# Kernel tuning notes

Hardware: AMD Instinct MI355X
Metric: run time of the kernel (lower is better)

Reference implementation:

```python
import jax, jax.numpy as jnp
import numpy as np

N_HEAD = 16
N_KV = 4
HEAD_DIM = 128
N_EMBD = 2048
GATE_CH = 32


def setup_inputs() -> dict:
    key = jax.random.key(0)
    ks = jax.random.split(key, 9)
    B, T = 2, 2048
    return {
        "x": jax.random.normal(ks[0], (B, T, N_EMBD), jnp.float32),
        "ve": jax.random.normal(ks[1], (B, T, N_KV * HEAD_DIM), jnp.float32),
        "cos": jax.random.uniform(ks[2], (T, 1, HEAD_DIM // 2), jnp.float32),
        "sin": jax.random.uniform(ks[3], (T, 1, HEAD_DIM // 2), jnp.float32),
        "wq": jax.random.normal(ks[4], (N_HEAD * HEAD_DIM, N_EMBD), jnp.float32) * 0.02,
        "wk": jax.random.normal(ks[5], (N_KV * HEAD_DIM, N_EMBD), jnp.float32) * 0.02,
        "wv": jax.random.normal(ks[6], (N_KV * HEAD_DIM, N_EMBD), jnp.float32) * 0.02,
        "wo": jax.random.normal(ks[7], (N_EMBD, N_EMBD), jnp.float32) * 0.02,
        "wgate": jax.random.normal(ks[8], (N_KV, GATE_CH), jnp.float32) * 0.02,
        "window_size": 512,
    }


def _rope(t, cos, sin):
    half = t.shape[-1] // 2
    t1, t2 = t[..., :half], t[..., half:]
    return jnp.concatenate([t1 * cos + t2 * sin, -t1 * sin + t2 * cos], axis=-1)


def _rms(t):
    eps = jnp.finfo(t.dtype).eps
    return t * jax.lax.rsqrt(jnp.mean(t * t, axis=-1, keepdims=True) + eps)


def reference(x, ve, cos, sin, wq, wk, wv, wo, wgate, window_size):
    B, T, _ = x.shape
    q = (x @ wq.T).reshape(B, T, N_HEAD, HEAD_DIM)
    k = (x @ wk.T).reshape(B, T, N_KV, HEAD_DIM)
    v = (x @ wv.T).reshape(B, T, N_KV, HEAD_DIM)
    # value-embedding gate
    gate = 2.0 * jax.nn.sigmoid(x[..., :GATE_CH] @ wgate.T)  # [B,T,N_KV]
    v = v + gate[..., None] * ve.reshape(B, T, N_KV, HEAD_DIM)
    # RoPE then QK RMSNorm
    q = _rms(_rope(q, cos, sin)).transpose(0, 2, 1, 3)  # [B,H,T,D]
    k = _rms(_rope(k, cos, sin)).transpose(0, 2, 1, 3)  # [B,KV,T,D]
    v = v.transpose(0, 2, 1, 3)
    rep = N_HEAD // N_KV
    k = jnp.repeat(k, rep, axis=1)  # repeat_interleave over head dim
    v = jnp.repeat(v, rep, axis=1)
    # sliding-window causal mask (past_len=0, key_len=T)
    pos = jnp.arange(T)
    mask = (pos[None, :] <= pos[:, None]) & (pos[None, :] >= pos[:, None] - window_size + 1)
    scale = 1.0 / jnp.sqrt(jnp.float32(HEAD_DIM))
    scores = jnp.einsum("bhqd,bhkd->bhqk", q, k) * scale
    scores = jnp.where(mask[None, None], scores, jnp.finfo(scores.dtype).min)
    attn = jax.nn.softmax(scores, axis=-1)
    y = jnp.einsum("bhqk,bhkd->bhqd", attn, v)
    y = y.transpose(0, 2, 1, 3).reshape(B, T, N_EMBD)
    return y @ wo.T
```

## Files before the change

kernel.cpp:

```cpp
#include <hip/hip_runtime.h>
#include <hip/hip_bf16.h>

typedef __attribute__((ext_vector_type(8))) short short8_t;
typedef __attribute__((ext_vector_type(4))) float f32x4;
typedef __attribute__((ext_vector_type(16))) float f32x16;
using bf16 = __hip_bfloat16;

#define MFMA_BF16(A, B, C) __builtin_amdgcn_mfma_f32_16x16x32_bf16((A), (B), (C), 0, 0, 0)
#define MFMA32_BF16(A, B, C) __builtin_amdgcn_mfma_f32_32x32x16_bf16((A), (B), (C), 0, 0, 0)

#define GLD_LDS16(g, l)                                                        \
  __builtin_amdgcn_global_load_lds(                                           \
      (const __attribute__((address_space(1))) unsigned int*)(const void*)(g),\
      (__attribute__((address_space(3))) unsigned int*)(void*)(l), 16, 0, 0)

__device__ __forceinline__ float bits2f(short s) {
  union { unsigned int u; float f; } c;
  c.u = ((unsigned int)(unsigned short)s) << 16;
  return c.f;
}
__device__ __forceinline__ short f2bits(float f) {
  bf16 h = __float2bfloat16(f);
  return *reinterpret_cast<short*>(&h);
}
__device__ __forceinline__ unsigned pack2(float lo, float hi) {
  return ((unsigned)(unsigned short)f2bits(lo)) |
         (((unsigned)(unsigned short)f2bits(hi)) << 16);
}
__device__ __forceinline__ float exp2_(float x) {
#if __has_builtin(__builtin_amdgcn_exp2f)
  return __builtin_amdgcn_exp2f(x);
#else
  return exp2f(x);
#endif
}

__global__ __launch_bounds__(256) void cvt_all(const float* __restrict__ x,
                                               const float* __restrict__ wq,
                                               const float* __restrict__ wk,
                                               const float* __restrict__ wv,
                                               const float* __restrict__ wo,
                                               short* __restrict__ xb,
                                               short* __restrict__ wqkvb,
                                               short* __restrict__ wob) {
  int i = (blockIdx.x * 256 + threadIdx.x) * 4;
  const float* src;
  short* dst;
  if (i < 8388608) {
    src = x + i; dst = xb + i;
  } else if (i < 14680064) {
    int j = i - 8388608;
    dst = wqkvb + j;
    if (j < 4194304) src = wq + j;
    else if (j < 5242880) src = wk + (j - 4194304);
    else src = wv + (j - 5242880);
  } else {
    int j = i - 14680064;
    src = wo + j; dst = wob + j;
  }
  float4 v = *reinterpret_cast<const float4*>(src);
  short4 o;
  o.x = f2bits(v.x); o.y = f2bits(v.y); o.z = f2bits(v.z); o.w = f2bits(v.w);
  *reinterpret_cast<short4*>(dst) = o;
}

template <int STORE_BF16>
__global__ __launch_bounds__(256, 2) void gemm_bt4(const short* __restrict__ A,
                                                   const short* __restrict__ Bt,
                                                   void* __restrict__ C,
                                                   int M, int N, int K,
                                                   int CM, int CN) {
  __shared__ __align__(16) short lds[2 * 16384];
  const int c = (int)blockIdx.x & 7;
  const int i = (int)blockIdx.x >> 3;
  const int cmi = c & 3, cni = c >> 2;
  const int m0 = (cmi * CM + (i % CM)) * 128;
  const int n0 = (cni * CN + (i / CM)) * 128;

  const int tid = threadIdx.x, w = tid >> 6, lane = tid & 63;
  const int wr = w >> 1, wc = w & 1;
  const int rr = lane & 15, g = lane >> 4;

  const int srow = tid >> 3;
  const int gc = (tid & 7) ^ (srow & 7);
  const short* Asrc = A + (size_t)(m0 + srow) * K + gc * 8;
  const short* Bsrc = Bt + (size_t)(n0 + srow) * K + gc * 8;
  const size_t rstep = (size_t)32 * K;
  const int dofs = tid * 16;

  const int abase = (((wr * 64 + rr) << 7) | (g << 4)) ^ ((rr & 7) << 4);
  const int bbase = ((((wc * 64 + rr) << 7) | (g << 4)) ^ ((rr & 7) << 4)) + 16384;

  f32x4 acc[4][4];
#pragma unroll
  for (int mi = 0; mi < 4; ++mi)
#pragma unroll
    for (int ni = 0; ni < 4; ++ni) acc[mi][ni] = (f32x4){0.f, 0.f, 0.f, 0.f};

  const int nt = K >> 6;

#define STAGE4(t, bufbyte) do {                                                \
    const short* a_ = Asrc + (size_t)(t) * 64;                                 \
    const short* b_ = Bsrc + (size_t)(t) * 64;                                 \
    char* la_ = (char*)lds + (bufbyte) + dofs;                                 \
    GLD_LDS16(a_,             la_);                                            \
    GLD_LDS16(a_ + rstep,     la_ + 4096);                                     \
    GLD_LDS16(a_ + 2 * rstep, la_ + 8192);                                     \
    GLD_LDS16(a_ + 3 * rstep, la_ + 12288);                                    \
    GLD_LDS16(b_,             la_ + 16384);                                    \
    GLD_LDS16(b_ + rstep,     la_ + 20480);                                    \
    GLD_LDS16(b_ + 2 * rstep, la_ + 24576);                                    \
    GLD_LDS16(b_ + 3 * rstep, la_ + 28672);                                    \
  } while (0)

  STAGE4(0, 0);
  asm volatile("s_waitcnt vmcnt(0)" ::: "memory");
  asm volatile("s_barrier" ::: "memory");

  int cur = 0;
  for (int t = 0; t < nt; ++t) {
    if (t + 1 < nt) STAGE4(t + 1, cur ^ 32768);
    const char* bufp = (const char*)lds + cur;
#pragma unroll
    for (int kk = 0; kk < 2; ++kk) {
      const int ko = kk * 64;
      short8_t a0 = *(const short8_t*)(bufp + ((abase ^ ko)));
      short8_t a1 = *(const short8_t*)(bufp + ((abase ^ ko) + 2048));
      short8_t a2 = *(const short8_t*)(bufp + ((abase ^ ko) + 4096));
      short8_t a3 = *(const short8_t*)(bufp + ((abase ^ ko) + 6144));
      short8_t b0 = *(const short8_t*)(bufp + ((bbase ^ ko)));
      short8_t b1 = *(const short8_t*)(bufp + ((bbase ^ ko) + 2048));
      short8_t b2 = *(const short8_t*)(bufp + ((bbase ^ ko) + 4096));
      short8_t b3 = *(const short8_t*)(bufp + ((bbase ^ ko) + 6144));
      __builtin_amdgcn_s_setprio(1);
      acc[0][0] = MFMA_BF16(a0, b0, acc[0][0]);
      acc[0][1] = MFMA_BF16(a0, b1, acc[0][1]);
      acc[0][2] = MFMA_BF16(a0, b2, acc[0][2]);
      acc[0][3] = MFMA_BF16(a0, b3, acc[0][3]);
      acc[1][0] = MFMA_BF16(a1, b0, acc[1][0]);
      acc[1][1] = MFMA_BF16(a1, b1, acc[1][1]);
      acc[1][2] = MFMA_BF16(a1, b2, acc[1][2]);
      acc[1][3] = MFMA_BF16(a1, b3, acc[1][3]);
      acc[2][0] = MFMA_BF16(a2, b0, acc[2][0]);
      acc[2][1] = MFMA_BF16(a2, b1, acc[2][1]);
      acc[2][2] = MFMA_BF16(a2, b2, acc[2][2]);
      acc[2][3] = MFMA_BF16(a2, b3, acc[2][3]);
      acc[3][0] = MFMA_BF16(a3, b0, acc[3][0]);
      acc[3][1] = MFMA_BF16(a3, b1, acc[3][1]);
      acc[3][2] = MFMA_BF16(a3, b2, acc[3][2]);
      acc[3][3] = MFMA_BF16(a3, b3, acc[3][3]);
      __builtin_amdgcn_s_setprio(0);
    }
    if (t + 1 < nt) {
      asm volatile("s_waitcnt vmcnt(0)" ::: "memory");
      asm volatile("s_barrier" ::: "memory");
    }
    cur ^= 32768;
  }
#undef STAGE4

#pragma unroll
  for (int mi = 0; mi < 4; ++mi)
#pragma unroll
    for (int ni = 0; ni < 4; ++ni) {
      const int row = m0 + wr * 64 + mi * 16 + g * 4;
      const int col = n0 + wc * 64 + ni * 16 + rr;
#pragma unroll
      for (int j = 0; j < 4; ++j) {
        float v = acc[mi][ni][j];
        if (STORE_BF16)
          reinterpret_cast<short*>(C)[(size_t)(row + j) * N + col] = f2bits(v);
        else
          reinterpret_cast<float*>(C)[(size_t)(row + j) * N + col] = v;
      }
    }
}

__global__ __launch_bounds__(256) void rope_rms_qk(const short* __restrict__ qkv,
                                                   const float* __restrict__ cosT,
                                                   const float* __restrict__ sinT,
                                                   short* __restrict__ qO,
                                                   short* __restrict__ kO) {
  const int T = 2048;
  int unit = blockIdx.x * 4 + (threadIdx.x >> 6);
  int lane = threadIdx.x & 63;
  int hh = unit % 20;
  int t = (unit / 20) % T;
  int b = unit / (20 * T);
  int col = hh < 16 ? hh * 128 : 2048 + (hh - 16) * 128;
  const short* src = qkv + (size_t)(b * T + t) * 3072 + col;
  float t1 = bits2f(src[lane]), t2 = bits2f(src[lane + 64]);
  float c = cosT[t * 64 + lane], s = sinT[t * 64 + lane];
  float o1 = t1 * c + t2 * s;
  float o2 = t2 * c - t1 * s;
  float ss = o1 * o1 + o2 * o2;
#pragma unroll
  for (int o = 1; o < 64; o <<= 1) ss += __shfl_xor(ss, o, 64);
  float r = rsqrtf(ss * (1.f / 128.f) + 1.1920929e-07f);
  short* dst;
  if (hh < 16) {
    r *= 0.08838834764831845f * 1.4426950408889634f;
    dst = qO + ((size_t)(b * 16 + hh) * T + t) * 128;
  } else {
    dst = kO + ((size_t)(b * 4 + (hh - 16)) * T + t) * 128;
  }
  dst[lane] = f2bits(o1 * r);
  dst[lane + 64] = f2bits(o2 * r);
}

__global__ __launch_bounds__(256) void vgate_t(const short* __restrict__ qkv,
                                               const float* __restrict__ x,
                                               const float* __restrict__ ve,
                                               const float* __restrict__ wgate,
                                               short* __restrict__ vT) {
  const int T = 2048;
  int bkv = blockIdx.x & 7;
  int t0 = (blockIdx.x >> 3) * 64;
  int b = bkv >> 2, kv = bkv & 3;
  __shared__ __align__(16) short L[128 * 64];
  int tid = threadIdx.x;
  int tt = tid >> 2, q = tid & 3;
  size_t m = (size_t)b * T + t0 + tt;
  float z = 0.f;
  const float* xp = x + m * 2048 + q * 8;
  const float* wgp = wgate + kv * 32 + q * 8;
#pragma unroll
  for (int i = 0; i < 8; ++i) z += xp[i] * wgp[i];
  z += __shfl_xor(z, 1, 64);
  z += __shfl_xor(z, 2, 64);
  float gate = 2.f / (1.f + __expf(-z));
  const short* vsrc = qkv + m * 3072 + 2560 + kv * 128 + q * 32;
  const float* vesrc = ve + m * 512 + kv * 128 + q * 32;
  short8_t v0 = *(const short8_t*)(vsrc);
  short8_t v1 = *(const short8_t*)(vsrc + 8);
  short8_t v2 = *(const short8_t*)(vsrc + 16);
  short8_t v3 = *(const short8_t*)(vsrc + 24);
  float4 e[8];
#pragma unroll
  for (int i = 0; i < 8; ++i) e[i] = *(const float4*)(vesrc + i * 4);
#pragma unroll
  for (int i = 0; i < 32; ++i) {
    int d = q * 32 + i;
    short vv = i < 8 ? v0[i] : i < 16 ? v1[i - 8] : i < 24 ? v2[i - 16] : v3[i - 24];
    float ev = (&e[i >> 2].x)[i & 3];
    int byte = (d * 128 + tt * 2) ^ ((d & 7) << 4);
    *(short*)((char*)L + byte) = f2bits(bits2f(vv) + gate * ev);
  }
  __syncthreads();
  int d = tid >> 1, th = tid & 1;
  const char* Lp = (const char*)L;
#pragma unroll
  for (int g2 = 0; g2 < 4; ++g2) {
    short8_t o = *(const short8_t*)(Lp + ((d * 128 + th * 64 + g2 * 16) ^ ((d & 7) << 4)));
    *(short8_t*)(vT + ((size_t)bkv * 128 + d) * T + t0 + th * 32 + g2 * 8) = o;
  }
}

__global__ __launch_bounds__(256) void attn_sw3(const short* __restrict__ Q,
                                                const short* __restrict__ K,
                                                const short* __restrict__ VT,
                                                short* __restrict__ Y,
                                                const int* __restrict__ winp) {
  const int T = 2048, H = 16;
  const int win = *winp;
  int combo = blockIdx.x & 7;
  int j = blockIdx.x >> 3;
  int b = combo >> 2, kvh = combo & 3;
  int h = kvh * 4 + (j & 3);
  int q0 = (15 - (j >> 2)) * 128;

  __shared__ __align__(16) short Ks[2][64 * 128];
  __shared__ __align__(16) short Vs[2][128 * 64];

  int tid = threadIdx.x, w = tid >> 6, lane = tid & 63;
  int ql = lane & 31, hi = lane >> 5;
  int qrow = q0 + w * 32 + ql;

  const short* qbase = Q + ((size_t)(b * H + h) * T + qrow) * 128;
  short8_t qf[8];
#pragma unroll
  for (int ks = 0; ks < 8; ++ks)
    qf[ks] = *reinterpret_cast<const short8_t*>(qbase + ks * 16 + hi * 8);

  const short* kbase = K + (size_t)(b * 4 + kvh) * T * 128;
  const short* vtbase = VT + (size_t)(b * 4 + kvh) * 128 * T;

  f32x16 acc[4];
#pragma unroll
  for (int dt = 0; dt < 4; ++dt)
#pragma unroll
    for (int r = 0; r < 16; ++r) acc[dt][r] = 0.f;
  float mreg = -1e30f, lsum = 0.f;

  int lo = q0 - win + 1;
  if (lo < 0) lo = 0;
  lo &= ~63;
  const int nt = (q0 + 128 - lo) >> 6;
  int qmin = q0 + w * 32, qmax = qmin + 31;

#define STAGE_A(ti, bi) do {                                                   \
    int kc_ = lo + (ti) * 64;                                                  \
    _Pragma("unroll")                                                          \
    for (int r = 0; r < 4; ++r) {                                              \
      int slot = (r * 4 + w) * 64 + lane;                                      \
      int krow = slot >> 4;                                                    \
      int gc = (slot & 15) ^ (krow & 7);                                       \
      GLD_LDS16(kbase + (size_t)(kc_ + krow) * 128 + gc * 8,                   \
                (char*)Ks[bi] + (r * 4 + w) * 1024);                           \
    }                                                                          \
    _Pragma("unroll")                                                          \
    for (int r = 0; r < 4; ++r) {                                              \
      int slot = (r * 4 + w) * 64 + lane;                                      \
      int d_ = slot >> 3;                                                      \
      int gc = (slot & 7) ^ (d_ & 7);                                          \
      GLD_LDS16(vtbase + (size_t)d_ * T + kc_ + gc * 8,                        \
                (char*)Vs[bi] + (r * 4 + w) * 1024);                           \
    }                                                                          \
  } while (0)

  STAGE_A(0, 0);

  int cur = 0;
  for (int t = 0; t < nt; ++t) {
    if (t + 1 < nt) {
      STAGE_A(t + 1, cur ^ 1);
      asm volatile("s_waitcnt vmcnt(8)" ::: "memory");
    } else {
      asm volatile("s_waitcnt vmcnt(0)" ::: "memory");
    }
    asm volatile("s_barrier" ::: "memory");

    int kc = lo + t * 64;
    bool active = (kc <= qmax) && (kc + 63 >= qmin - win + 1);
    if (active) {
      const char* Kp = (const char*)Ks[cur];
      const char* Vp = (const char*)Vs[cur];
      f32x16 sA[2];
#pragma unroll
      for (int r = 0; r < 16; ++r) { sA[0][r] = 0.f; sA[1][r] = 0.f; }
#pragma unroll
      for (int kt = 0; kt < 2; ++kt) {
        int kr = kt * 32 + ql;
#pragma unroll
        for (int ks = 0; ks < 8; ++ks) {
          int byte = kr * 256 + (((ks * 2 + hi) ^ (kr & 7)) << 4);
          short8_t kf = *reinterpret_cast<const short8_t*>(Kp + byte);
          sA[kt] = MFMA32_BF16(kf, qf[ks], sA[kt]);
        }
      }
      float pmax = -1e30f;
#pragma unroll
      for (int kt = 0; kt < 2; ++kt)
#pragma unroll
        for (int r = 0; r < 16; ++r) {
          int key = kc + kt * 32 + (r & 3) + 8 * (r >> 2) + 4 * hi;
          float sv = sA[kt][r];
          sv = ((unsigned)(qrow - key) < (unsigned)win) ? sv : -1e30f;
          sA[kt][r] = sv;
          pmax = fmaxf(pmax, sv);
        }
      pmax = fmaxf(pmax, __shfl_xor(pmax, 32, 64));
      float mn = fmaxf(mreg, pmax);
      float corr = exp2_(mreg - mn);
      mreg = mn;
      float rs = 0.f;
#pragma unroll
      for (int kt = 0; kt < 2; ++kt)
#pragma unroll
        for (int r = 0; r < 16; ++r) {
          float p = exp2_(sA[kt][r] - mn);
          sA[kt][r] = p;
          rs += p;
        }
      rs += __shfl_xor(rs, 32, 64);
      lsum = lsum * corr + rs;
#pragma unroll
      for (int dt = 0; dt < 4; ++dt)
#pragma unroll
        for (int r = 0; r < 16; ++r) acc[dt][r] *= corr;

#pragma unroll
      for (int kt = 0; kt < 2; ++kt)
#pragma unroll
        for (int s = 0; s < 2; ++s) {
          unsigned a = pack2(sA[kt][8 * s + 0], sA[kt][8 * s + 1]);
          unsigned bb = pack2(sA[kt][8 * s + 2], sA[kt][8 * s + 3]);
          unsigned c = pack2(sA[kt][8 * s + 4], sA[kt][8 * s + 5]);
          unsigned dd = pack2(sA[kt][8 * s + 6], sA[kt][8 * s + 7]);
          unsigned sa = __shfl_xor(a, 32, 64);
          unsigned sb = __shfl_xor(bb, 32, 64);
          unsigned sc2 = __shfl_xor(c, 32, 64);
          unsigned sd = __shfl_xor(dd, 32, 64);
          union { unsigned u[4]; short8_t s8; } pu;
          pu.u[0] = hi ? sc2 : a;
          pu.u[1] = hi ? sd : bb;
          pu.u[2] = hi ? c : sa;
          pu.u[3] = hi ? dd : sb;
          const int kst = kt * 2 + s;
#pragma unroll
          for (int dt = 0; dt < 4; ++dt) {
            int d_ = dt * 32 + ql;
            int byte = (d_ << 7) + ((((kst * 2 + hi)) ^ (d_ & 7)) << 4);
            short8_t vf = *reinterpret_cast<const short8_t*>(Vp + byte);
            acc[dt] = MFMA32_BF16(vf, pu.s8, acc[dt]);
          }
        }
    }
    asm volatile("s_barrier" ::: "memory");
    cur ^= 1;
  }
#undef STAGE_A

  float rinv = 1.f / lsum;
  short* ybase = Y + ((size_t)(b * T + qrow) * H + h) * 128;
#pragma unroll
  for (int dt = 0; dt < 4; ++dt)
#pragma unroll
    for (int g2 = 0; g2 < 4; ++g2) {
      short4 o;
      o.x = f2bits(acc[dt][g2 * 4 + 0] * rinv);
      o.y = f2bits(acc[dt][g2 * 4 + 1] * rinv);
      o.z = f2bits(acc[dt][g2 * 4 + 2] * rinv);
      o.w = f2bits(acc[dt][g2 * 4 + 3] * rinv);
      *reinterpret_cast<short4*>(ybase + dt * 32 + 8 * g2 + 4 * hi) = o;
    }
}

extern "C" void kernel_launch(void* const* d_in, const int* in_sizes, int n_in,
                              void* d_out, int out_size, void* d_ws, size_t ws_size,
                              hipStream_t stream) {
  const float* x = (const float*)d_in[0];
  const float* ve = (const float*)d_in[1];
  const float* cosT = (const float*)d_in[2];
  const float* sinT = (const float*)d_in[3];
  const float* wq = (const float*)d_in[4];
  const float* wk = (const float*)d_in[5];
  const float* wv = (const float*)d_in[6];
  const float* wo = (const float*)d_in[7];
  const float* wgate = (const float*)d_in[8];
  const int* winp = (const int*)d_in[9];
  float* out = (float*)d_out;
  char* ws = (char*)d_ws;

  const int B = 2, T = 2048;
  short* xb    = (short*)(ws);
  short* wqkvb = (short*)(ws + 16777216);
  short* wob   = (short*)(ws + 29360128);
  short* qkv   = (short*)(ws + 37748736);
  short* qpost = (short*)(ws + 62914560);
  short* kpost = (short*)(ws + 79691776);
  short* vTb   = (short*)(ws + 83886080);
  short* ybuf  = (short*)(ws + 88080384);

  cvt_all<<<dim3(18432), 256, 0, stream>>>(x, wq, wk, wv, wo, xb, wqkvb, wob);

  gemm_bt4<1><<<dim3(768), 256, 0, stream>>>(xb, wqkvb, qkv, 4096, 3072, 2048, 8, 12);

  rope_rms_qk<<<dim3(B * T * 20 / 4), 256, 0, stream>>>(qkv, cosT, sinT, qpost, kpost);
  vgate_t<<<dim3(8 * (T / 64)), 256, 0, stream>>>(qkv, x, ve, wgate, vTb);

  attn_sw3<<<dim3(512), 256, 0, stream>>>(qpost, kpost, vTb, ybuf, winp);

  gemm_bt4<0><<<dim3(512), 256, 0, stream>>>(ybuf, wob, out, 4096, 2048, 2048, 8, 8);
}
```

Measured before the change: 176.5 us.

## Fuse RoPE/RMSNorm and V gating/transpose into QKV GEMM epilogue

The QKV projection GEMM now does its post-processing in its epilogue. Each 128-column tile is one head, so RoPE plus RMSNorm for Q/K and the value-embedding gate plus transpose for V run directly on the accumulators, staged through LDS. This drops the intermediate bf16 qkv buffer and two extra kernel launches with their global round trips. In exchange, the fused template uses somewhat more shared memory, the epilogue is heavier and raises register pressure, and occupancy may drop.

```diff
diff --git a/kernel.cpp b/kernel.cpp
--- a/kernel.cpp
+++ b/kernel.cpp
@@ -64,13 +64,16 @@
   *reinterpret_cast<short4*>(dst) = o;
 }
 
-template <int STORE_BF16>
-__global__ __launch_bounds__(256, 2) void gemm_bt4(const short* __restrict__ A,
-                                                   const short* __restrict__ Bt,
-                                                   void* __restrict__ C,
-                                                   int M, int N, int K,
-                                                   int CM, int CN) {
-  __shared__ __align__(16) short lds[2 * 16384];
+template <int STORE_BF16, int FUSED>
+__global__ __launch_bounds__(256, 2) void gemm_bt4(
+    const short* __restrict__ A, const short* __restrict__ Bt,
+    void* __restrict__ C, int M, int N, int K, int CM, int CN,
+    short* __restrict__ qO, short* __restrict__ kO, short* __restrict__ vTO,
+    const float* __restrict__ cosT, const float* __restrict__ sinT,
+    const float* __restrict__ x32, const float* __restrict__ ve32,
+    const float* __restrict__ wg32) {
+  __shared__ __align__(16) char smem[FUSED ? 67584 : 65536];
+  short* lds = (short*)smem;
   const int c = (int)blockIdx.x & 7;
   const int i = (int)blockIdx.x >> 3;
   const int cmi = c & 3, cni = c >> 2;
@@ -159,100 +162,118 @@
   }
 #undef STAGE4
 
-#pragma unroll
-  for (int mi = 0; mi < 4; ++mi)
-#pragma unroll
-    for (int ni = 0; ni < 4; ++ni) {
-      const int row = m0 + wr * 64 + mi * 16 + g * 4;
-      const int col = n0 + wc * 64 + ni * 16 + rr;
-#pragma unroll
-      for (int j = 0; j < 4; ++j) {
-        float v = acc[mi][ni][j];
-        if (STORE_BF16)
-          reinterpret_cast<short*>(C)[(size_t)(row + j) * N + col] = f2bits(v);
-        else
-          reinterpret_cast<float*>(C)[(size_t)(row + j) * N + col] = v;
+  if (!FUSED) {
+#pragma unroll
+    for (int mi = 0; mi < 4; ++mi)
+#pragma unroll
+      for (int ni = 0; ni < 4; ++ni) {
+        const int row = m0 + wr * 64 + mi * 16 + g * 4;
+        const int col = n0 + wc * 64 + ni * 16 + rr;
+#pragma unroll
+        for (int j = 0; j < 4; ++j) {
+          float v = acc[mi][ni][j];
+          if (STORE_BF16)
+            reinterpret_cast<short*>(C)[(size_t)(row + j) * N + col] = f2bits(v);
+          else
+            reinterpret_cast<float*>(C)[(size_t)(row + j) * N + col] = v;
+        }
       }
-    }
-}
-
-__global__ __launch_bounds__(256) void rope_rms_qk(const short* __restrict__ qkv,
-                                                   const float* __restrict__ cosT,
-                                                   const float* __restrict__ sinT,
-                                                   short* __restrict__ qO,
-                                                   short* __restrict__ kO) {
-  const int T = 2048;
-  int unit = blockIdx.x * 4 + (threadIdx.x >> 6);
-  int lane = threadIdx.x & 63;
-  int hh = unit % 20;
-  int t = (unit / 20) % T;
-  int b = unit / (20 * T);
-  int col = hh < 16 ? hh * 128 : 2048 + (hh - 16) * 128;
-  const short* src = qkv + (size_t)(b * T + t) * 3072 + col;
-  float t1 = bits2f(src[lane]), t2 = bits2f(src[lane + 64]);
-  float c = cosT[t * 64 + lane], s = sinT[t * 64 + lane];
-  float o1 = t1 * c + t2 * s;
-  float o2 = t2 * c - t1 * s;
-  float ss = o1 * o1 + o2 * o2;
-#pragma unroll
-  for (int o = 1; o < 64; o <<= 1) ss += __shfl_xor(ss, o, 64);
-  float r = rsqrtf(ss * (1.f / 128.f) + 1.1920929e-07f);
-  short* dst;
-  if (hh < 16) {
-    r *= 0.08838834764831845f * 1.4426950408889634f;
-    dst = qO + ((size_t)(b * 16 + hh) * T + t) * 128;
+    return;
+  }
+
+  __syncthreads();
+  const int slot = n0 >> 7;
+
+  if (slot < 20) {
+    float* S = (float*)smem;
+#pragma unroll
+    for (int mi = 0; mi < 4; ++mi)
+#pragma unroll
+      for (int ni = 0; ni < 4; ++ni) {
+        int r0 = wr * 64 + mi * 16 + g * 4;
+        int cl = wc * 64 + ni * 16 + rr;
+#pragma unroll
+        for (int j = 0; j < 4; ++j) S[(r0 + j) * 132 + cl] = acc[mi][ni][j];
+      }
+    __syncthreads();
+    int row = tid >> 1, u = tid & 1;
+    int mglob = m0 + row;
+    int bb = mglob >> 11, tk = mglob & 2047;
+    const float* Sr = S + row * 132 + u * 32;
+    const float* cp = cosT + tk * 64 + u * 32;
+    const float* sp = sinT + tk * 64 + u * 32;
+    float o1[32], o2[32];
+    float ss = 0.f;
+#pragma unroll
+    for (int ii = 0; ii < 32; ++ii) {
+      float t1 = Sr[ii], t2 = Sr[ii + 64];
+      float cv = cp[ii], sv = sp[ii];
+      o1[ii] = t1 * cv + t2 * sv;
+      o2[ii] = t2 * cv - t1 * sv;
+      ss += o1[ii] * o1[ii] + o2[ii] * o2[ii];
+    }
+    ss += __shfl_xor(ss, 1, 64);
+    float r = rsqrtf(ss * (1.f / 128.f) + 1.1920929e-07f);
+    short* dst;
+    if (slot < 16) {
+      r *= 0.08838834764831845f * 1.4426950408889634f;
+      dst = qO + ((size_t)(bb * 16 + slot) * 2048 + tk) * 128 + u * 32;
+    } else {
+      dst = kO + ((size_t)(bb * 4 + (slot - 16)) * 2048 + tk) * 128 + u * 32;
+    }
+#pragma unroll
+    for (int v8 = 0; v8 < 4; ++v8) {
+      short8_t s1, s2;
+#pragma unroll
+      for (int k2 = 0; k2 < 8; ++k2) {
+        s1[k2] = f2bits(o1[v8 * 8 + k2] * r);
+        s2[k2] = f2bits(o2[v8 * 8 + k2] * r);
+      }
+      *(short8_t*)(dst + v8 * 8) = s1;
+      *(short8_t*)(dst + 64 + v8 * 8) = s2;
+    }
   } else {
-    dst = kO + ((size_t)(b * 4 + (hh - 16)) * T + t) * 128;
-  }
-  dst[lane] = f2bits(o1 * r);
-  dst[lane + 64] = f2bits(o2 * r);
-}
-
-__global__ __launch_bounds__(256) void vgate_t(const short* __restrict__ qkv,
-                                               const float* __restrict__ x,
-                                               const float* __restrict__ ve,
-                                               const float* __restrict__ wgate,
-                                               short* __restrict__ vT) {
-  const int T = 2048;
-  int bkv = blockIdx.x & 7;
-  int t0 = (blockIdx.x >> 3) * 64;
-  int b = bkv >> 2, kv = bkv & 3;
-  __shared__ __align__(16) short L[128 * 64];
-  int tid = threadIdx.x;
-  int tt = tid >> 2, q = tid & 3;
-  size_t m = (size_t)b * T + t0 + tt;
-  float z = 0.f;
-  const float* xp = x + m * 2048 + q * 8;
-  const float* wgp = wgate + kv * 32 + q * 8;
-#pragma unroll
-  for (int i = 0; i < 8; ++i) z += xp[i] * wgp[i];
-  z += __shfl_xor(z, 1, 64);
-  z += __shfl_xor(z, 2, 64);
-  float gate = 2.f / (1.f + __expf(-z));
-  const short* vsrc = qkv + m * 3072 + 2560 + kv * 128 + q * 32;
-  const float* vesrc = ve + m * 512 + kv * 128 + q * 32;
-  short8_t v0 = *(const short8_t*)(vsrc);
-  short8_t v1 = *(const short8_t*)(vsrc + 8);
-  short8_t v2 = *(const short8_t*)(vsrc + 16);
-  short8_t v3 = *(const short8_t*)(vsrc + 24);
-  float4 e[8];
-#pragma unroll
-  for (int i = 0; i < 8; ++i) e[i] = *(const float4*)(vesrc + i * 4);
-#pragma unroll
-  for (int i = 0; i < 32; ++i) {
-    int d = q * 32 + i;
-    short vv = i < 8 ? v0[i] : i < 16 ? v1[i - 8] : i < 24 ? v2[i - 16] : v3[i - 24];
-    float ev = (&e[i >> 2].x)[i & 3];
-    int byte = (d * 128 + tt * 2) ^ ((d & 7) << 4);
-    *(short*)((char*)L + byte) = f2bits(bits2f(vv) + gate * ev);
-  }
-  __syncthreads();
-  int d = tid >> 1, th = tid & 1;
-  const char* Lp = (const char*)L;
-#pragma unroll
-  for (int g2 = 0; g2 < 4; ++g2) {
-    short8_t o = *(const short8_t*)(Lp + ((d * 128 + th * 64 + g2 * 16) ^ ((d & 7) << 4)));
-    *(short8_t*)(vT + ((size_t)bkv * 128 + d) * T + t0 + th * 32 + g2 * 8) = o;
+    const int kv = slot - 20;
+    short* TL = (short*)smem;
+    float* GL = (float*)(smem + 32768);
+    {
+      int row = tid >> 1, u = tid & 1;
+      size_t mglob = (size_t)(m0 + row);
+      const float* xp = x32 + mglob * 2048 + u * 16;
+      const float* wg = wg32 + kv * 32 + u * 16;
+      float z = 0.f;
+#pragma unroll
+      for (int ii = 0; ii < 16; ++ii) z += xp[ii] * wg[ii];
+      z += __shfl_xor(z, 1, 64);
+      if (!u) GL[row] = 2.f / (1.f + __expf(-z));
+    }
+    __syncthreads();
+#pragma unroll
+    for (int mi = 0; mi < 4; ++mi)
+#pragma unroll
+      for (int ni = 0; ni < 4; ++ni) {
+        int r0 = wr * 64 + mi * 16 + g * 4;
+        int cl = wc * 64 + ni * 16 + rr;
+#pragma unroll
+        for (int j = 0; j < 4; ++j) {
+          int rw = r0 + j;
+          float gate = GL[rw];
+          float ev = ve32[(size_t)(m0 + rw) * 512 + kv * 128 + cl];
+          float v = acc[mi][ni][j] + gate * ev;
+          int byte = ((cl << 8) + (rw << 1)) ^ ((cl & 7) << 4);
+          *(short*)((char*)TL + byte) = f2bits(v);
+        }
+      }
+    __syncthreads();
+    int d = tid >> 1, th = tid & 1;
+    int bb = m0 >> 11, t0l = m0 & 2047;
+    short* vdst = vTO + ((size_t)(bb * 4 + kv) * 128 + d) * 2048 + t0l + th * 64;
+    const char* TLp = (const char*)TL;
+#pragma unroll
+    for (int g2 = 0; g2 < 8; ++g2) {
+      short8_t o = *(const short8_t*)(TLp + (((d << 8) + th * 128 + g2 * 16) ^ ((d & 7) << 4)));
+      *(short8_t*)(vdst + g2 * 8) = o;
+    }
   }
 }
 
@@ -446,7 +467,6 @@
   short* xb    = (short*)(ws);
   short* wqkvb = (short*)(ws + 16777216);
   short* wob   = (short*)(ws + 29360128);
-  short* qkv   = (short*)(ws + 37748736);
   short* qpost = (short*)(ws + 62914560);
   short* kpost = (short*)(ws + 79691776);
   short* vTb   = (short*)(ws + 83886080);
@@ -454,12 +474,13 @@
 
   cvt_all<<<dim3(18432), 256, 0, stream>>>(x, wq, wk, wv, wo, xb, wqkvb, wob);
 
-  gemm_bt4<1><<<dim3(768), 256, 0, stream>>>(xb, wqkvb, qkv, 4096, 3072, 2048, 8, 12);
-
-  rope_rms_qk<<<dim3(B * T * 20 / 4), 256, 0, stream>>>(qkv, cosT, sinT, qpost, kpost);
-  vgate_t<<<dim3(8 * (T / 64)), 256, 0, stream>>>(qkv, x, ve, wgate, vTb);
+  gemm_bt4<1, 1><<<dim3(768), 256, 0, stream>>>(
+      xb, wqkvb, nullptr, 4096, 3072, 2048, 8, 12,
+      qpost, kpost, vTb, cosT, sinT, x, ve, wgate);
 
   attn_sw3<<<dim3(512), 256, 0, stream>>>(qpost, kpost, vTb, ybuf, winp);
 
-  gemm_bt4<0><<<dim3(512), 256, 0, stream>>>(ybuf, wob, out, 4096, 2048, 2048, 8, 8);
-}
+  gemm_bt4<0, 0><<<dim3(512), 256, 0, stream>>>(
+      ybuf, wob, out, 4096, 2048, 2048, 8, 8,
+      nullptr, nullptr, nullptr, nullptr, nullptr, nullptr, nullptr, nullptr);
+}
```

Measured after the change: 164.4 us. 1.07x faster.

## Replace QKV projection GEMM with 256x256-tile 8-wave ping-pong kernel

Applied to the files above, without the earlier changes.

Adds a new bf16 GEMM kernel with 256x256 output tiles, 512 threads (8 waves), double-buffered LDS staging via direct global-to-LDS loads, and a four-phase schedule that interleaves LDS fragment reads and next-tile prefetches with MFMA bursts under raised wave priority. The QKV projection now uses this kernel with 192 workgroups instead of 768 128x128 tiles. The goal is more data reuse per LDS byte and better overlap of memory and compute. The trade-off is fewer workgroups than the 256 CUs, so some CUs sit idle, plus heavier register and LDS use (128 KB LDS per block).

```diff
diff --git a/kernel.cpp b/kernel.cpp
--- a/kernel.cpp
+++ b/kernel.cpp
@@ -62,6 +62,188 @@
   short4 o;
   o.x = f2bits(v.x); o.y = f2bits(v.y); o.z = f2bits(v.z); o.w = f2bits(v.w);
   *reinterpret_cast<short4*>(dst) = o;
+}
+
+template <int STORE_BF16>
+__global__ __launch_bounds__(512, 2) void gemm_8p(const short* __restrict__ A,
+                                                  const short* __restrict__ Bt,
+                                                  void* __restrict__ C,
+                                                  int M, int N, int K, int NBN) {
+  __shared__ __align__(16) short lds[2 * 32768];
+  const int nwg = gridDim.x;
+  const int cpx = nwg >> 3;
+  const int wg = ((int)blockIdx.x & 7) * cpx + ((int)blockIdx.x >> 3);
+  const int m0 = (wg / NBN) * 256, n0 = (wg % NBN) * 256;
+
+  const int tid = threadIdx.x, w = tid >> 6, lane = tid & 63;
+  const int wm = w >> 2, wn = w & 3;
+  const int rr = lane & 15, g = lane >> 4;
+
+  const int prow = tid >> 3;
+  const int lg = (tid & 7) ^ (prow & 7);
+  const size_t ro0 = (size_t)prow * K + lg * 8;
+  const size_t ro1 = ro0 + (size_t)64 * K;
+  const short* Ab = A + (size_t)m0 * K;
+  const short* Bb = Bt + (size_t)n0 * K;
+  const short* Ab1 = Ab + (size_t)128 * K;
+  const short* Bb1 = Bb + (size_t)128 * K;
+  const int wofs = tid * 16;
+
+#define STG8(bp, tt, regbuf) do {                                              \
+    const short* s_ = (bp) + (size_t)(tt) * 64;                                \
+    char* d_ = (char*)lds + (regbuf) + wofs;                                   \
+    GLD_LDS16(s_ + ro0, d_);                                                   \
+    GLD_LDS16(s_ + ro1, d_ + 8192);                                            \
+  } while (0)
+
+  const int xg0 = ((g ^ (rr & 7)) << 4);
+  const int xg1 = (((4 + g) ^ (rr & 7)) << 4);
+  const int aregion = wm * 16384;
+  const int bregion = 32768 + (wn >> 1) * 16384;
+  const int arow0 = rr * 128;
+  const int brow0 = ((wn & 1) * 64 + rr) * 128;
+
+  f32x4 acc[8][4];
+#pragma unroll
+  for (int i2 = 0; i2 < 8; ++i2)
+#pragma unroll
+    for (int jj = 0; jj < 4; ++jj) acc[i2][jj] = (f32x4){0.f, 0.f, 0.f, 0.f};
+
+  const int nt = K >> 6;
+
+  STG8(Ab, 0, 0);
+  STG8(Ab1, 0, 16384);
+  STG8(Bb, 0, 32768);
+  STG8(Bb1, 0, 49152);
+  if (nt > 1) {
+    STG8(Ab, 1, 65536);
+    STG8(Ab1, 1, 65536 + 16384);
+    STG8(Bb, 1, 65536 + 32768);
+    STG8(Bb1, 1, 65536 + 49152);
+    asm volatile("s_waitcnt vmcnt(8)" ::: "memory");
+  } else {
+    asm volatile("s_waitcnt vmcnt(0)" ::: "memory");
+  }
+  asm volatile("s_barrier" ::: "memory");
+
+  short8_t aF[4][2], b0F[2][2], b1F[2][2];
+
+  for (int t = 0; t < nt; ++t) {
+    const int bb = (t & 1) << 16;
+    const char* L = (const char*)lds;
+    const bool st2 = (t + 2) < nt;
+
+#pragma unroll
+    for (int mi = 0; mi < 4; ++mi) {
+      int rb = bb + aregion + arow0 + mi * 2048;
+      aF[mi][0] = *(const short8_t*)(L + rb + xg0);
+      aF[mi][1] = *(const short8_t*)(L + rb + xg1);
+    }
+#pragma unroll
+    for (int ni = 0; ni < 2; ++ni) {
+      int rb = bb + bregion + brow0 + ni * 2048;
+      b0F[ni][0] = *(const short8_t*)(L + rb + xg0);
+      b0F[ni][1] = *(const short8_t*)(L + rb + xg1);
+    }
+    asm volatile("s_barrier" ::: "memory");
+    asm volatile("s_waitcnt lgkmcnt(0)" ::: "memory");
+    __builtin_amdgcn_sched_barrier(0);
+    __builtin_amdgcn_s_setprio(1);
+#pragma unroll
+    for (int kk = 0; kk < 2; ++kk)
+#pragma unroll
+      for (int mi = 0; mi < 4; ++mi)
+#pragma unroll
+        for (int ni = 0; ni < 2; ++ni)
+          acc[mi][ni] = MFMA_BF16(aF[mi][kk], b0F[ni][kk], acc[mi][ni]);
+    __builtin_amdgcn_s_setprio(0);
+    asm volatile("s_barrier" ::: "memory");
+
+#pragma unroll
+    for (int ni = 0; ni < 2; ++ni) {
+      int rb = bb + bregion + brow0 + 4096 + ni * 2048;
+      b1F[ni][0] = *(const short8_t*)(L + rb + xg0);
+      b1F[ni][1] = *(const short8_t*)(L + rb + xg1);
+    }
+    asm volatile("s_barrier" ::: "memory");
+    asm volatile("s_waitcnt lgkmcnt(0)" ::: "memory");
+    __builtin_amdgcn_sched_barrier(0);
+    __builtin_amdgcn_s_setprio(1);
+#pragma unroll
+    for (int kk = 0; kk < 2; ++kk)
+#pragma unroll
+      for (int mi = 0; mi < 4; ++mi)
+#pragma unroll
+        for (int ni = 0; ni < 2; ++ni)
+          acc[mi][2 + ni] = MFMA_BF16(aF[mi][kk], b1F[ni][kk], acc[mi][2 + ni]);
+    __builtin_amdgcn_s_setprio(0);
+    asm volatile("s_barrier" ::: "memory");
+
+#pragma unroll
+    for (int mi = 0; mi < 4; ++mi) {
+      int rb = bb + aregion + arow0 + 8192 + mi * 2048;
+      aF[mi][0] = *(const short8_t*)(L + rb + xg0);
+      aF[mi][1] = *(const short8_t*)(L + rb + xg1);
+    }
+    if (st2) {
+      STG8(Bb, t + 2, bb + 32768);
+      STG8(Bb1, t + 2, bb + 49152);
+    }
+    asm volatile("s_barrier" ::: "memory");
+    asm volatile("s_waitcnt lgkmcnt(0)" ::: "memory");
+    __builtin_amdgcn_sched_barrier(0);
+    __builtin_amdgcn_s_setprio(1);
+#pragma unroll
+    for (int kk = 0; kk < 2; ++kk)
+#pragma unroll
+      for (int mi = 0; mi < 4; ++mi)
+#pragma unroll
+        for (int ni = 0; ni < 2; ++ni)
+          acc[4 + mi][2 + ni] = MFMA_BF16(aF[mi][kk], b1F[ni][kk], acc[4 + mi][2 + ni]);
+    __builtin_amdgcn_s_setprio(0);
+    asm volatile("s_barrier" ::: "memory");
+
+    if (st2) {
+      STG8(Ab, t + 2, bb + 0);
+      STG8(Ab1, t + 2, bb + 16384);
+    }
+    asm volatile("s_barrier" ::: "memory");
+    __builtin_amdgcn_s_setprio(1);
+#pragma unroll
+    for (int kk = 0; kk < 2; ++kk)
+#pragma unroll
+      for (int mi = 0; mi < 4; ++mi)
+#pragma unroll
+        for (int ni = 0; ni < 2; ++ni)
+          acc[4 + mi][ni] = MFMA_BF16(aF[mi][kk], b0F[ni][kk], acc[4 + mi][ni]);
+    __builtin_amdgcn_s_setprio(0);
+    if (st2)
+      asm volatile("s_waitcnt vmcnt(8)" ::: "memory");
+    else if (t + 1 < nt)
+      asm volatile("s_waitcnt vmcnt(0)" ::: "memory");
+    asm volatile("s_barrier" ::: "memory");
+  }
+#undef STG8
+
+#pragma unroll
+  for (int mh = 0; mh < 2; ++mh)
+#pragma unroll
+    for (int mi = 0; mi < 4; ++mi)
+#pragma unroll
+      for (int nh = 0; nh < 2; ++nh)
+#pragma unroll
+        for (int ni = 0; ni < 2; ++ni) {
+          const int row = m0 + wm * 128 + mh * 64 + mi * 16 + g * 4;
+          const int col = n0 + wn * 64 + nh * 32 + ni * 16 + rr;
+          f32x4 v = acc[mh * 4 + mi][nh * 2 + ni];
+#pragma unroll
+          for (int j = 0; j < 4; ++j) {
+            if (STORE_BF16)
+              reinterpret_cast<short*>(C)[(size_t)(row + j) * N + col] = f2bits(v[j]);
+            else
+              reinterpret_cast<float*>(C)[(size_t)(row + j) * N + col] = v[j];
+          }
+        }
 }
 
 template <int STORE_BF16>
@@ -454,7 +636,7 @@
 
   cvt_all<<<dim3(18432), 256, 0, stream>>>(x, wq, wk, wv, wo, xb, wqkvb, wob);
 
-  gemm_bt4<1><<<dim3(768), 256, 0, stream>>>(xb, wqkvb, qkv, 4096, 3072, 2048, 8, 12);
+  gemm_8p<1><<<dim3(192), 512, 0, stream>>>(xb, wqkvb, qkv, 4096, 3072, 2048, 12);
 
   rope_rms_qk<<<dim3(B * T * 20 / 4), 256, 0, stream>>>(qkv, cosT, sinT, qpost, kpost);
   vgate_t<<<dim3(8 * (T / 64)), 256, 0, stream>>>(qkv, x, ve, wgate, vTb);
```

Result: slower. 184.7 us (+4.6%).
